# Kernel optimization log

Hardware: AMD Instinct MI355X
Metric: run time of the kernel (lower is better)

## Reference

```python
import jax, jax.numpy as jnp
import numpy as np

NLAT, NLON = 361, 720
LMAX = NLAT               # equiangular grid: lmax = nlat
MMAX = NLON // 2 + 1      # mmax = nlon//2 + 1
B, C = 1, 128


def _precompute_legpoly(mmax, lmax, t, csphase=True):
    """Associated Legendre vandermonde P_l^m(cos t), orthonormal, inverse=True
    (norm factor 1 for 'ortho'). Shape [mmax, lmax, nlat]. Setup-time numpy only."""
    x = np.cos(t)
    nmax = max(mmax, lmax)
    vdm = np.zeros((nmax, nmax, len(x)))
    vdm[0, 0] = np.sqrt(1.0 / (4.0 * np.pi))
    for l in range(1, nmax):
        vdm[l - 1, l] = np.sqrt(2 * l + 1) * x * vdm[l - 1, l - 1]
        vdm[l, l] = np.sqrt((2 * l + 1) * (1 + x) * (1 - x) / (2 * l)) * vdm[l - 1, l - 1]
    for l in range(2, nmax):
        for m in range(l - 1):
            a = np.sqrt((2 * l - 1) / (l - m) * (2 * l + 1) / (l + m))
            b = np.sqrt((l + m - 1) / (l - m) * (2 * l + 1) / (2 * l - 3) * (l - m - 1) / (l + m))
            vdm[m, l] = a * x * vdm[m, l - 1] - b * vdm[m, l - 2]
    vdm = vdm[:mmax, :lmax]
    if csphase:
        vdm[1::2] *= -1.0  # Condon-Shortley phase on odd m
    return vdm


def setup_inputs() -> dict:
    key = jax.random.key(0)
    # spherical harmonic coefficients as real view: [B, C, lmax, mmax, 2]
    x_real = jax.random.normal(key, (B, C, LMAX, MMAX, 2), dtype=jnp.float32)
    # equiangular (Clenshaw-Curtiss) colatitudes, t = flip(arccos(cos(pi*j/(n-1))))
    t = np.pi * np.arange(NLAT) / (NLAT - 1)
    pct = jnp.asarray(_precompute_legpoly(MMAX, LMAX, t), dtype=jnp.float32)  # [mmax, lmax, nlat]
    return {"x_real": x_real, "pct": pct}


def reference(x_real, pct):
    # single-device case: comm sizes == 1, all distributed transposes are identity
    # and nlatpad == nlonpad == 0.
    # per-m triangular Legendre contraction over l (torch einsum '...lmr,mlk->...kmr')
    xs = jnp.einsum('bclmr,mlk->bckmr', x_real, pct)        # [B, C, nlat, mmax, 2]
    xc = jax.lax.complex(xs[..., 0], xs[..., 1])            # [B, C, nlat, mmax]
    # inverse real FFT along longitude, norm='forward' (no 1/n scaling on inverse)
    out = jnp.fft.irfft(xc, n=NLON, axis=-1, norm='forward')  # [B, C, nlat, nlon]
    return out.astype(x_real.dtype)
```

## Files before the change

### kernel.cpp

```cpp
#include <hip/hip_runtime.h>
#include <cstddef>

#define CC   128
#define LDIM 361
#define MDIM 361
#define KDIM 361
#define NLON 720
#define LP   384
#define KP   384
#define KTP  384
#define MRP  736
#define NP   768
#define CK   (CC*KDIM)
#define CR   (2*CC)

typedef __attribute__((ext_vector_type(8))) short short8;
typedef __attribute__((ext_vector_type(4))) float floatx4;

__device__ __forceinline__ unsigned short f2bf(float f) {
    union { float f; unsigned u; } v; v.f = f;
    unsigned u = v.u;
    u += 0x7fffu + ((u >> 16) & 1u);
    return (unsigned short)(u >> 16);
}

__device__ __forceinline__ void async_copy16(const void* g, void* l) {
    __builtin_amdgcn_global_load_lds(
        (const __attribute__((address_space(1))) void*)g,
        (__attribute__((address_space(3))) void*)l, 16, 0, 0);
}

__device__ __forceinline__ int xcd_swz(int id, int P) {
    int x = id & 7, g = id >> 3;
    int q = P >> 3, r = P & 7;
    int start = (x < r) ? x * (q + 1) : r * (q + 1) + (x - r) * q;
    return start + g;
}

__global__ void sht_gen_T(unsigned short* __restrict__ Tp) {
    int idx = blockIdx.x * 256 + threadIdx.x;
    if (idx >= NP * MRP) return;
    int n = idx / MRP, mr = idx - n * MRP;
    float v = 0.f;
    if (n < NLON && mr < 2 * MDIM) {
        int m = mr >> 1, im = mr & 1;
        if (m == 0)            v = im ? 0.f : 1.f;
        else if (m == MDIM-1)  v = im ? 0.f : ((n & 1) ? -1.f : 1.f);
        else {
            int ph = (m * n) % NLON;
            float ang = (float)ph * (float)(3.14159265358979323846 / 360.0);
            v = im ? (-2.f * sinf(ang)) : (2.f * cosf(ang));
        }
    }
    Tp[idx] = f2bf(v);
}

__global__ __launch_bounds__(256)
void sht_prep_x(const float* __restrict__ x, unsigned short* __restrict__ xA) {
    __shared__ float2 tile[64][33];
    const int mt = blockIdx.x;
    const int lt = blockIdx.y;
    const int c  = blockIdx.z;
    const int t  = threadIdx.x;

    #pragma unroll
    for (int u = 0; u < 8; ++u) {
        int p  = t + 256 * u;
        int li = p >> 5, mi = p & 31;
        int l = lt * 64 + li, m = mt * 32 + mi;
        float2 v = make_float2(0.f, 0.f);
        if (l < LDIM && m < MDIM)
            v = *(const float2*)(x + ((size_t)(c * LDIM + l) * MDIM + m) * 2);
        tile[li][mi] = v;
    }
    __syncthreads();

    #pragma unroll
    for (int u = 0; u < 2; ++u) {
        int s  = t + 256 * u;
        int mi = s >> 4, rr = (s >> 3) & 1, lo = (s & 7) * 8;
        int m = mt * 32 + mi;
        if (m >= MDIM) continue;
        short8 h;
        #pragma unroll
        for (int e = 0; e < 8; ++e) {
            float2 p = tile[lo + e][mi];
            h[e] = (short)f2bf(rr ? p.y : p.x);
        }
        *(short8*)(xA + ((size_t)m * CR + 2 * c + rr) * LP + lt * 64 + lo) = h;
    }
}

__global__ __launch_bounds__(256)
void sht_prep_pct(const float* __restrict__ pct, unsigned short* __restrict__ pctT) {
    __shared__ float tile[32][33];
    const int m  = blockIdx.y;
    const int kt = blockIdx.x % 12;
    const int lt = blockIdx.x / 12;
    const int l0 = lt * 32, k0 = kt * 32;
    const int t  = threadIdx.x;

    const int ki = t & 31, lbase = t >> 5;
    #pragma unroll
    for (int u = 0; u < 4; ++u) {
        int li = lbase + 8 * u;
        int l = l0 + li, k = k0 + ki;
        float v = 0.f;
        if (l < LDIM && k < KDIM)
            v = pct[((size_t)m * LDIM + l) * KDIM + k];
        tile[li][ki] = v;
    }
    __syncthreads();

    const int ko = t >> 3, lo = (t & 7) * 4;
    unsigned pk0 = (unsigned)f2bf(tile[lo + 0][ko]) | ((unsigned)f2bf(tile[lo + 1][ko]) << 16);
    unsigned pk1 = (unsigned)f2bf(tile[lo + 2][ko]) | ((unsigned)f2bf(tile[lo + 3][ko]) << 16);
    unsigned* dst = (unsigned*)(pctT + ((size_t)m * KP + k0 + ko) * LP + l0 + lo);
    dst[0] = pk0; dst[1] = pk1;
}

__global__ __launch_bounds__(512)
void sht_stageA4(const unsigned short* __restrict__ pctT, const unsigned short* __restrict__ xA,
                 unsigned short* __restrict__ xsT) {
    __shared__ unsigned short As[2][128 * 32];
    __shared__ unsigned short Bs[2][384 * 32];

    const int p   = xcd_swz(blockIdx.x, 2 * MDIM);
    const int m   = p >> 1, ct = p & 1;
    const int c0  = ct * 128;
    const int t   = threadIdx.x;
    const int w   = t >> 6, L = t & 63;
    const int wr  = w & 1, wc = w >> 1;
    const int lane15 = L & 15, quad = L >> 4;
    const int arr = t >> 2, alq = t & 3;

    const unsigned short* xAm = xA + (size_t)m * CR * LP;
    const unsigned short* pTm = pctT + (size_t)m * KP * LP;

    floatx4 acc[4][6] = {};

    auto stage = [&](int buf, int kb) {
        async_copy16(xAm + (size_t)(c0 + arr) * LP + kb + alq * 8,
                     &As[buf][(w * 64) * 8]);
        #pragma unroll
        for (int u = 0; u < 3; ++u) {
            int s = u * 512 + t;
            int rr = s >> 2, lq = s & 3;
            async_copy16(pTm + (size_t)rr * LP + kb + lq * 8,
                         &Bs[buf][(u * 512 + w * 64) * 8]);
        }
    };

    const int NT = LP / 32;
    stage(0, 0);
    __syncthreads();

    int cur = 0;
    for (int it = 0; it < NT; ++it) {
        if (it + 1 < NT) stage(cur ^ 1, (it + 1) * 32);

        short8 af[4], bf[6];
        #pragma unroll
        for (int i = 0; i < 4; ++i)
            af[i] = *(const short8*)&As[cur][((wr * 64 + i * 16 + lane15) * 4 + quad) * 8];
        #pragma unroll
        for (int j = 0; j < 6; ++j)
            bf[j] = *(const short8*)&Bs[cur][((wc * 96 + j * 16 + lane15) * 4 + quad) * 8];
        __builtin_amdgcn_s_setprio(1);
        #pragma unroll
        for (int i = 0; i < 4; ++i)
            #pragma unroll
            for (int j = 0; j < 6; ++j)
                acc[i][j] = __builtin_amdgcn_mfma_f32_16x16x32_bf16(af[i], bf[j], acc[i][j], 0, 0, 0);
        __builtin_amdgcn_s_setprio(0);
        __syncthreads();
        cur ^= 1;
    }

    #pragma unroll
    for (int i = 0; i < 4; ++i) {
        #pragma unroll
        for (int j = 0; j < 6; ++j) {
            int k = wc * 96 + j * 16 + lane15;
            #pragma unroll
            for (int e = 0; e < 4; ++e) {
                int cr = c0 + wr * 64 + i * 16 + quad * 4 + e;
                xsT[((size_t)m * CR + cr) * KTP + k] = f2bf(acc[i][j][e]);
            }
        }
    }
}

__global__ __launch_bounds__(256)
void sht_xs_tr(const unsigned short* __restrict__ xsT, unsigned short* __restrict__ xs) {
    __shared__ unsigned short tile[128 * 65];
    const int c  = blockIdx.y;
    const int bx = blockIdx.x;
    const int mt = bx / 6, kt = bx % 6;
    const int m0 = mt * 64, k0 = kt * 64;
    const int t  = threadIdx.x;

    #pragma unroll
    for (int u = 0; u < 4; ++u) {
        int q = t + 256 * u;
        int rho = q >> 3, ko8 = q & 7;
        int mi = rho >> 1, r = rho & 1;
        int m = m0 + mi;
        short8 v = {};
        if (m < MDIM)
            v = *(const short8*)(xsT + ((size_t)m * CR + 2 * c + r) * KTP + k0 + ko8 * 8);
        *(short8*)&tile[rho * 65 + ko8 * 8] = v;
    }
    __syncthreads();

    #pragma unroll
    for (int u = 0; u < 4; ++u) {
        int q = t + 256 * u;
        int kk = q >> 4, mc = q & 15;
        int k = k0 + kk;
        int mr0 = 2 * m0 + mc * 8;
        if (k >= KDIM || mr0 >= MRP) continue;
        short8 h;
        #pragma unroll
        for (int e = 0; e < 8; ++e)
            h[e] = (short)tile[(mc * 8 + e) * 65 + kk];
        *(short8*)(xs + (size_t)(c * KDIM + k) * MRP + mr0) = h;
    }
}

__global__ __launch_bounds__(512)
void sht_stageA2(const unsigned short* __restrict__ pctT, const unsigned short* __restrict__ xA,
                 unsigned short* __restrict__ xs) {
    __shared__ unsigned short As[128 * 32];
    __shared__ unsigned short Bs[384 * 32];

    const int p   = xcd_swz(blockIdx.x, 2 * MDIM);
    const int m   = p >> 1, ct = p & 1;
    const int c0  = ct * 128;
    const int t   = threadIdx.x;
    const int w   = t >> 6, L = t & 63;
    const int wr  = w & 1, wc = w >> 1;
    const int lane15 = L & 15, quad = L >> 4;
    const int arr = t >> 2, alq = t & 3;

    const unsigned short* xAm = xA + (size_t)m * CR * LP;
    const unsigned short* pTm = pctT + (size_t)m * KP * LP;

    floatx4 acc[4][6] = {};

    for (int kb = 0; kb < LP; kb += 32) {
        async_copy16(xAm + (size_t)(c0 + arr) * LP + kb + alq * 8,
                     As + (size_t)(w * 64) * 8);
        #pragma unroll
        for (int u = 0; u < 3; ++u) {
            int s = u * 512 + t;
            int rr = s >> 2, lq = s & 3;
            async_copy16(pTm + (size_t)rr * LP + kb + lq * 8,
                         Bs + (size_t)(u * 512 + w * 64) * 8);
        }
        __syncthreads();

        short8 af[4], bf[6];
        #pragma unroll
        for (int i = 0; i < 4; ++i)
            af[i] = *(const short8*)&As[((wr * 64 + i * 16 + lane15) * 4 + quad) * 8];
        #pragma unroll
        for (int j = 0; j < 6; ++j)
            bf[j] = *(const short8*)&Bs[((wc * 96 + j * 16 + lane15) * 4 + quad) * 8];
        #pragma unroll
        for (int i = 0; i < 4; ++i)
            #pragma unroll
            for (int j = 0; j < 6; ++j)
                acc[i][j] = __builtin_amdgcn_mfma_f32_16x16x32_bf16(af[i], bf[j], acc[i][j], 0, 0, 0);
        __syncthreads();
    }

    #pragma unroll
    for (int j = 0; j < 6; ++j) {
        int k = wc * 96 + j * 16 + lane15;
        if (k >= KDIM) continue;
        #pragma unroll
        for (int i = 0; i < 4; ++i) {
            #pragma unroll
            for (int eh = 0; eh < 2; ++eh) {
                int cr = c0 + wr * 64 + i * 16 + quad * 4 + eh * 2;
                int c  = cr >> 1;
                unsigned pack = (unsigned)f2bf(acc[i][j][eh * 2]) |
                                ((unsigned)f2bf(acc[i][j][eh * 2 + 1]) << 16);
                *(unsigned*)(xs + (size_t)(c * KDIM + k) * MRP + 2 * m) = pack;
            }
        }
    }
}

__global__ __launch_bounds__(256)
void sht_stageA(const float* __restrict__ pct, const unsigned short* __restrict__ xA,
                unsigned short* __restrict__ xs) {
    __shared__ unsigned short As[128 * 32];
    __shared__ unsigned short Bs[32 * 130];

    const int m   = blockIdx.y;
    const int ct  = blockIdx.x & 1;
    const int kt  = blockIdx.x >> 1;
    const int c0  = ct * 128;
    const int n0  = kt * 128;
    const int t   = threadIdx.x;
    const int w   = t >> 6, L = t & 63;
    const int wr  = w & 1, wc = w >> 1;
    const int lane15 = L & 15, quad = L >> 4;
    const int bl = t >> 3, bkq = t & 7;

    const unsigned short* xAm = xA + (size_t)m * CR * LP;
    const float* pctm = pct + (size_t)m * LDIM * KDIM;

    floatx4 acc[4][4] = {};

    for (int kb = 0; kb < LP; kb += 32) {
        #pragma unroll
        for (int i = 0; i < 2; ++i) {
            int s = w * 128 + i * 64 + L;
            int cr = s >> 2, lq = s & 3;
            async_copy16(xAm + (size_t)(c0 + cr) * LP + kb + lq * 8,
                         As + (size_t)(w * 128 + i * 64) * 8);
        }
        {
            int l = kb + bl;
            bool lok = (l < LDIM);
            const float* prow = pctm + (size_t)l * KDIM;
            #pragma unroll
            for (int u = 0; u < 4; ++u) {
                int kc = n0 + u * 32 + bkq * 4;
                float f0 = (lok && kc + 0 < KDIM) ? prow[kc + 0] : 0.f;
                float f1 = (lok && kc + 1 < KDIM) ? prow[kc + 1] : 0.f;
                float f2 = (lok && kc + 2 < KDIM) ? prow[kc + 2] : 0.f;
                float f3 = (lok && kc + 3 < KDIM) ? prow[kc + 3] : 0.f;
                unsigned* bp = (unsigned*)&Bs[bl * 130 + u * 32 + bkq * 4];
                bp[0] = (unsigned)f2bf(f0) | ((unsigned)f2bf(f1) << 16);
                bp[1] = (unsigned)f2bf(f2) | ((unsigned)f2bf(f3) << 16);
            }
        }
        __syncthreads();

        short8 af[4];
        #pragma unroll
        for (int i = 0; i < 4; ++i) {
            int row = wr * 64 + i * 16 + lane15;
            af[i] = *(const short8*)&As[(row * 4 + quad) * 8];
        }
        #pragma unroll
        for (int jf = 0; jf < 4; ++jf) {
            int col = wc * 64 + jf * 16 + lane15;
            short8 bf;
            #pragma unroll
            for (int j = 0; j < 8; ++j)
                bf[j] = (short)Bs[(quad * 8 + j) * 130 + col];
            #pragma unroll
            for (int i = 0; i < 4; ++i)
                acc[i][jf] = __builtin_amdgcn_mfma_f32_16x16x32_bf16(af[i], bf, acc[i][jf], 0, 0, 0);
        }
        __syncthreads();
    }

    #pragma unroll
    for (int i = 0; i < 4; ++i) {
        #pragma unroll
        for (int jf = 0; jf < 4; ++jf) {
            int k = n0 + wc * 64 + jf * 16 + lane15;
            if (k >= KDIM) continue;
            #pragma unroll
            for (int eh = 0; eh < 2; ++eh) {
                int cr = c0 + wr * 64 + i * 16 + quad * 4 + eh * 2;
                int c  = cr >> 1;
                unsigned pack = (unsigned)f2bf(acc[i][jf][eh * 2]) |
                                ((unsigned)f2bf(acc[i][jf][eh * 2 + 1]) << 16);
                *(unsigned*)(xs + (size_t)(c * KDIM + k) * MRP + 2 * m) = pack;
            }
        }
    }
}

__global__ __launch_bounds__(512)
void sht_stageB3(const unsigned short* __restrict__ xs, const unsigned short* __restrict__ Tp,
                 float* __restrict__ out) {
    __shared__ unsigned short As[2][128 * 32];
    __shared__ unsigned short Bs[2][384 * 32];

    const int p   = xcd_swz(blockIdx.x, 2 * MDIM);
    const int ckt = p >> 1, nt = p & 1;
    const int ck0 = ckt * 128, n0 = nt * 384;
    const int t   = threadIdx.x;
    const int w   = t >> 6, L = t & 63;
    const int wr  = w & 1, wc = w >> 1;
    const int lane15 = L & 15, quad = L >> 4;
    const int arr = t >> 2, alq = t & 3;

    floatx4 acc[4][6] = {};

    auto stage = [&](int buf, int kb) {
        async_copy16(xs + (size_t)(ck0 + arr) * MRP + kb + alq * 8,
                     &As[buf][(w * 64) * 8]);
        #pragma unroll
        for (int u = 0; u < 3; ++u) {
            int s = u * 512 + t;
            int rr = s >> 2, lq = s & 3;
            async_copy16(Tp + (size_t)(n0 + rr) * MRP + kb + lq * 8,
                         &Bs[buf][(u * 512 + w * 64) * 8]);
        }
    };

    const int NT = MRP / 32;
    stage(0, 0);
    __syncthreads();

    int cur = 0;
    for (int it = 0; it < NT; ++it) {
        if (it + 1 < NT) stage(cur ^ 1, (it + 1) * 32);

        short8 af[4], bf[6];
        #pragma unroll
        for (int i = 0; i < 4; ++i)
            af[i] = *(const short8*)&As[cur][((wr * 64 + i * 16 + lane15) * 4 + quad) * 8];
        #pragma unroll
        for (int j = 0; j < 6; ++j)
            bf[j] = *(const short8*)&Bs[cur][((wc * 96 + j * 16 + lane15) * 4 + quad) * 8];
        __builtin_amdgcn_s_setprio(1);
        #pragma unroll
        for (int i = 0; i < 4; ++i)
            #pragma unroll
            for (int j = 0; j < 6; ++j)
                acc[i][j] = __builtin_amdgcn_mfma_f32_16x16x32_bf16(af[i], bf[j], acc[i][j], 0, 0, 0);
        __builtin_amdgcn_s_setprio(0);
        __syncthreads();
        cur ^= 1;
    }

    #pragma unroll
    for (int i = 0; i < 4; ++i) {
        int ckr = ck0 + wr * 64 + i * 16 + quad * 4;
        #pragma unroll
        for (int j = 0; j < 6; ++j) {
            int jj = n0 + wc * 96 + j * 16 + lane15;
            if (jj >= NLON) continue;
            #pragma unroll
            for (int e = 0; e < 4; ++e)
                out[(size_t)(ckr + e) * NLON + jj] = acc[i][j][e];
        }
    }
}

extern "C" void kernel_launch(void* const* d_in, const int* in_sizes, int n_in,
                              void* d_out, int out_size, void* d_ws, size_t ws_size,
                              hipStream_t stream) {
    const float* x   = (const float*)d_in[0];
    const float* pct = (const float*)d_in[1];
    float* out = (float*)d_out;

    unsigned short* xs = (unsigned short*)d_ws;
    unsigned short* Tp = xs + (size_t)CK * MRP;
    unsigned short* xA = (unsigned short*)d_out;

    const size_t base_shorts = (size_t)CK * MRP + (size_t)NP * MRP;
    const size_t pctT_shorts = (size_t)MDIM * KP * LP;
    const size_t xsT_shorts  = (size_t)MDIM * CR * KTP;
    const bool fast1 = ws_size >= (base_shorts + pctT_shorts) * sizeof(unsigned short);
    const bool fast2 = ws_size >= (base_shorts + pctT_shorts + xsT_shorts) * sizeof(unsigned short);

    sht_gen_T<<<(NP * MRP + 255) / 256, 256, 0, stream>>>(Tp);
    sht_prep_x<<<dim3(12, 6, 128), 256, 0, stream>>>(x, xA);
    if (fast2) {
        unsigned short* pctT = Tp + (size_t)NP * MRP;
        unsigned short* xsT  = pctT + pctT_shorts;
        sht_prep_pct<<<dim3(144, MDIM), 256, 0, stream>>>(pct, pctT);
        sht_stageA4<<<dim3(2 * MDIM), 512, 0, stream>>>(pctT, xA, xsT);
        sht_xs_tr<<<dim3(36, 128), 256, 0, stream>>>(xsT, xs);
    } else if (fast1) {
        unsigned short* pctT = Tp + (size_t)NP * MRP;
        sht_prep_pct<<<dim3(144, MDIM), 256, 0, stream>>>(pct, pctT);
        sht_stageA2<<<dim3(2 * MDIM), 512, 0, stream>>>(pctT, xA, xs);
    } else {
        sht_stageA<<<dim3(6, MDIM), 256, 0, stream>>>(pct, xA, xs);
    }
    sht_stageB3<<<dim3(2 * MDIM), 512, 0, stream>>>(xs, Tp, out);
}
```

Before: 626.7 us.

## Triple-buffer GEMM stages with vmcnt waits and repack transpose tiles

Both MFMA GEMM kernels (stage A and stage B) move from double-buffered LDS staging with two __syncthreads per iteration to a three-deep ring. Each iteration waits with a partial s_waitcnt vmcnt and issues a single s_barrier, so two tiles of global loads stay in flight while MFMAs run. The transpose kernels (prep_x and xs_tr) also change their LDS layouts: real and imaginary parts are split into separate planes, and bf16 pairs are packed into 32-bit words so reads and writes are wider and bank conflicts fewer. Triple buffering raises LDS use per block, about 96KB, which may lower occupancy. The hand-written vmcnt count of 4 must exactly match the number of async copies issued per stage, otherwise a tile can be read before it arrives.

```diff
diff --git a/kernel.cpp b/kernel.cpp
--- a/kernel.cpp
+++ b/kernel.cpp
@@ -57,7 +57,7 @@
 
 __global__ __launch_bounds__(256)
 void sht_prep_x(const float* __restrict__ x, unsigned short* __restrict__ xA) {
-    __shared__ float2 tile[64][33];
+    __shared__ float tp[2][32 * 65 + 4];
     const int mt = blockIdx.x;
     const int lt = blockIdx.y;
     const int c  = blockIdx.z;
@@ -71,7 +71,8 @@
         float2 v = make_float2(0.f, 0.f);
         if (l < LDIM && m < MDIM)
             v = *(const float2*)(x + ((size_t)(c * LDIM + l) * MDIM + m) * 2);
-        tile[li][mi] = v;
+        tp[0][mi * 65 + li] = v.x;
+        tp[1][mi * 65 + li] = v.y;
     }
     __syncthreads();
 
@@ -81,12 +82,11 @@
         int mi = s >> 4, rr = (s >> 3) & 1, lo = (s & 7) * 8;
         int m = mt * 32 + mi;
         if (m >= MDIM) continue;
+        const float* pl = &tp[rr][mi * 65];
         short8 h;
         #pragma unroll
-        for (int e = 0; e < 8; ++e) {
-            float2 p = tile[lo + e][mi];
-            h[e] = (short)f2bf(rr ? p.y : p.x);
-        }
+        for (int e = 0; e < 8; ++e)
+            h[e] = (short)f2bf(pl[lo + e]);
         *(short8*)(xA + ((size_t)m * CR + 2 * c + rr) * LP + lt * 64 + lo) = h;
     }
 }
@@ -120,10 +120,10 @@
 }
 
 __global__ __launch_bounds__(512)
-void sht_stageA4(const unsigned short* __restrict__ pctT, const unsigned short* __restrict__ xA,
+void sht_stageA5(const unsigned short* __restrict__ pctT, const unsigned short* __restrict__ xA,
                  unsigned short* __restrict__ xsT) {
-    __shared__ unsigned short As[2][128 * 32];
-    __shared__ unsigned short Bs[2][384 * 32];
+    __shared__ unsigned short As[3][128 * 32];
+    __shared__ unsigned short Bs[3][384 * 32];
 
     const int p   = xcd_swz(blockIdx.x, 2 * MDIM);
     const int m   = p >> 1, ct = p & 1;
@@ -153,19 +153,23 @@
 
     const int NT = LP / 32;
     stage(0, 0);
-    __syncthreads();
-
-    int cur = 0;
+    stage(1, 32);
+
     for (int it = 0; it < NT; ++it) {
-        if (it + 1 < NT) stage(cur ^ 1, (it + 1) * 32);
+        const int cb = it % 3;
+        if (it + 1 < NT) { asm volatile("s_waitcnt vmcnt(4)" ::: "memory"); }
+        else             { asm volatile("s_waitcnt vmcnt(0)" ::: "memory"); }
+        __builtin_amdgcn_sched_barrier(0);
+        __builtin_amdgcn_s_barrier();
+        __builtin_amdgcn_sched_barrier(0);
 
         short8 af[4], bf[6];
         #pragma unroll
         for (int i = 0; i < 4; ++i)
-            af[i] = *(const short8*)&As[cur][((wr * 64 + i * 16 + lane15) * 4 + quad) * 8];
+            af[i] = *(const short8*)&As[cb][((wr * 64 + i * 16 + lane15) * 4 + quad) * 8];
         #pragma unroll
         for (int j = 0; j < 6; ++j)
-            bf[j] = *(const short8*)&Bs[cur][((wc * 96 + j * 16 + lane15) * 4 + quad) * 8];
+            bf[j] = *(const short8*)&Bs[cb][((wc * 96 + j * 16 + lane15) * 4 + quad) * 8];
         __builtin_amdgcn_s_setprio(1);
         #pragma unroll
         for (int i = 0; i < 4; ++i)
@@ -173,8 +177,8 @@
             for (int j = 0; j < 6; ++j)
                 acc[i][j] = __builtin_amdgcn_mfma_f32_16x16x32_bf16(af[i], bf[j], acc[i][j], 0, 0, 0);
         __builtin_amdgcn_s_setprio(0);
-        __syncthreads();
-        cur ^= 1;
+
+        if (it + 2 < NT) stage((it + 2) % 3, (it + 2) * 32);
     }
 
     #pragma unroll
@@ -193,7 +197,7 @@
 
 __global__ __launch_bounds__(256)
 void sht_xs_tr(const unsigned short* __restrict__ xsT, unsigned short* __restrict__ xs) {
-    __shared__ unsigned short tile[128 * 65];
+    __shared__ unsigned tile32[64 * 65];
     const int c  = blockIdx.y;
     const int bx = blockIdx.x;
     const int mt = bx / 6, kt = bx % 6;
@@ -201,30 +205,36 @@
     const int t  = threadIdx.x;
 
     #pragma unroll
+    for (int u = 0; u < 2; ++u) {
+        int q  = t + 256 * u;
+        int mi = q >> 3, ko8 = q & 7;
+        int m  = m0 + mi;
+        short8 a = {}, b = {};
+        if (m < MDIM) {
+            const unsigned short* base = xsT + ((size_t)m * CR + 2 * c) * KTP + k0 + ko8 * 8;
+            a = *(const short8*)base;
+            b = *(const short8*)(base + KTP);
+        }
+        #pragma unroll
+        for (int e = 0; e < 8; ++e)
+            tile32[(ko8 * 8 + e) * 65 + mi] =
+                (unsigned)(unsigned short)a[e] | ((unsigned)(unsigned short)b[e] << 16);
+    }
+    __syncthreads();
+
+    #pragma unroll
     for (int u = 0; u < 4; ++u) {
-        int q = t + 256 * u;
-        int rho = q >> 3, ko8 = q & 7;
-        int mi = rho >> 1, r = rho & 1;
-        int m = m0 + mi;
-        short8 v = {};
-        if (m < MDIM)
-            v = *(const short8*)(xsT + ((size_t)m * CR + 2 * c + r) * KTP + k0 + ko8 * 8);
-        *(short8*)&tile[rho * 65 + ko8 * 8] = v;
-    }
-    __syncthreads();
-
-    #pragma unroll
-    for (int u = 0; u < 4; ++u) {
-        int q = t + 256 * u;
+        int q  = t + 256 * u;
         int kk = q >> 4, mc = q & 15;
-        int k = k0 + kk;
+        int k  = k0 + kk;
         int mr0 = 2 * m0 + mc * 8;
         if (k >= KDIM || mr0 >= MRP) continue;
-        short8 h;
-        #pragma unroll
-        for (int e = 0; e < 8; ++e)
-            h[e] = (short)tile[(mc * 8 + e) * 65 + kk];
-        *(short8*)(xs + (size_t)(c * KDIM + k) * MRP + mr0) = h;
+        unsigned w0 = tile32[kk * 65 + mc * 4 + 0];
+        unsigned w1 = tile32[kk * 65 + mc * 4 + 1];
+        unsigned w2 = tile32[kk * 65 + mc * 4 + 2];
+        unsigned w3 = tile32[kk * 65 + mc * 4 + 3];
+        unsigned* dst = (unsigned*)(xs + (size_t)(c * KDIM + k) * MRP + mr0);
+        dst[0] = w0; dst[1] = w1; dst[2] = w2; dst[3] = w3;
     }
 }
 
@@ -380,10 +390,10 @@
 }
 
 __global__ __launch_bounds__(512)
-void sht_stageB3(const unsigned short* __restrict__ xs, const unsigned short* __restrict__ Tp,
+void sht_stageB4(const unsigned short* __restrict__ xs, const unsigned short* __restrict__ Tp,
                  float* __restrict__ out) {
-    __shared__ unsigned short As[2][128 * 32];
-    __shared__ unsigned short Bs[2][384 * 32];
+    __shared__ unsigned short As[3][128 * 32];
+    __shared__ unsigned short Bs[3][384 * 32];
 
     const int p   = xcd_swz(blockIdx.x, 2 * MDIM);
     const int ckt = p >> 1, nt = p & 1;
@@ -410,19 +420,23 @@
 
     const int NT = MRP / 32;
     stage(0, 0);
-    __syncthreads();
-
-    int cur = 0;
+    stage(1, 32);
+
     for (int it = 0; it < NT; ++it) {
-        if (it + 1 < NT) stage(cur ^ 1, (it + 1) * 32);
+        const int cb = it % 3;
+        if (it + 1 < NT) { asm volatile("s_waitcnt vmcnt(4)" ::: "memory"); }
+        else             { asm volatile("s_waitcnt vmcnt(0)" ::: "memory"); }
+        __builtin_amdgcn_sched_barrier(0);
+        __builtin_amdgcn_s_barrier();
+        __builtin_amdgcn_sched_barrier(0);
 
         short8 af[4], bf[6];
         #pragma unroll
         for (int i = 0; i < 4; ++i)
-            af[i] = *(const short8*)&As[cur][((wr * 64 + i * 16 + lane15) * 4 + quad) * 8];
+            af[i] = *(const short8*)&As[cb][((wr * 64 + i * 16 + lane15) * 4 + quad) * 8];
         #pragma unroll
         for (int j = 0; j < 6; ++j)
-            bf[j] = *(const short8*)&Bs[cur][((wc * 96 + j * 16 + lane15) * 4 + quad) * 8];
+            bf[j] = *(const short8*)&Bs[cb][((wc * 96 + j * 16 + lane15) * 4 + quad) * 8];
         __builtin_amdgcn_s_setprio(1);
         #pragma unroll
         for (int i = 0; i < 4; ++i)
@@ -430,8 +444,8 @@
             for (int j = 0; j < 6; ++j)
                 acc[i][j] = __builtin_amdgcn_mfma_f32_16x16x32_bf16(af[i], bf[j], acc[i][j], 0, 0, 0);
         __builtin_amdgcn_s_setprio(0);
-        __syncthreads();
-        cur ^= 1;
+
+        if (it + 2 < NT) stage((it + 2) % 3, (it + 2) * 32);
     }
 
     #pragma unroll
@@ -471,7 +485,7 @@
         unsigned short* pctT = Tp + (size_t)NP * MRP;
         unsigned short* xsT  = pctT + pctT_shorts;
         sht_prep_pct<<<dim3(144, MDIM), 256, 0, stream>>>(pct, pctT);
-        sht_stageA4<<<dim3(2 * MDIM), 512, 0, stream>>>(pctT, xA, xsT);
+        sht_stageA5<<<dim3(2 * MDIM), 512, 0, stream>>>(pctT, xA, xsT);
         sht_xs_tr<<<dim3(36, 128), 256, 0, stream>>>(xsT, xs);
     } else if (fast1) {
         unsigned short* pctT = Tp + (size_t)NP * MRP;
@@ -480,5 +494,5 @@
     } else {
         sht_stageA<<<dim3(6, MDIM), 256, 0, stream>>>(pct, xA, xs);
     }
-    sht_stageB3<<<dim3(2 * MDIM), 512, 0, stream>>>(xs, Tp, out);
-}
+    sht_stageB4<<<dim3(2 * MDIM), 512, 0, stream>>>(xs, Tp, out);
+}
```

Result: faster. 601.5 us (-4.0%).
